# Kernel optimization log

Hardware: AMD Instinct MI355X
Metric: run time of the kernel (lower is better)

## Reference

```python
import jax, jax.numpy as jnp
import numpy as np

N_E = 50000
N_R = 1000
E = 800000
E_HIDDEN = 256
R_HIDDEN = 64
NEG_SLOPE = 0.01  # torch F.leaky_relu default


def segment_softmax(logits, seg, num_segments):
    # numerically stable per-segment softmax over edges
    seg_max = jax.ops.segment_max(logits, seg, num_segments=num_segments)
    seg_max = jnp.where(jnp.isfinite(seg_max), seg_max, 0.0)
    ex = jnp.exp(logits - seg_max[seg])
    denom = jax.ops.segment_sum(ex, seg, num_segments=num_segments)
    return ex / (denom[seg] + 1e-16)


def setup_inputs() -> dict:
    key = jax.random.key(0)
    ks = jax.random.split(key, 9)
    return {
        "x_e": jax.random.normal(ks[0], (N_E, E_HIDDEN), dtype=jnp.float32),
        "x_r": jax.random.normal(ks[1], (N_R, R_HIDDEN), dtype=jnp.float32),
        "edge_index": jax.random.randint(ks[2], (2, E), 0, N_E, dtype=jnp.int64),
        "rel": jax.random.randint(ks[3], (E,), 0, N_R, dtype=jnp.int64),
        "line_graph_index": jax.random.randint(ks[4], (2, E), 0, E, dtype=jnp.int64),
        "line_graph_val": jax.random.uniform(ks[5], (E,), dtype=jnp.float32),
        "a_h_w": jax.random.normal(ks[6], (E_HIDDEN,), dtype=jnp.float32),
        "a_t_w": jax.random.normal(ks[7], (E_HIDDEN,), dtype=jnp.float32),
        "a_r_w": jax.random.normal(ks[8], (R_HIDDEN,), dtype=jnp.float32),
    }


def reference(x_e, x_r, edge_index, rel, line_graph_index, line_graph_val, a_h_w, a_t_w, a_r_w):
    head, tail = edge_index[0], edge_index[1]
    # per-node scalar scores, gathered per edge
    s_e_h = jnp.einsum("nd,d->n", x_e, a_h_w)  # [N_e]
    s_e_t = jnp.einsum("nd,d->n", x_e, a_t_w)  # [N_e]
    s_r = jnp.einsum("rd,d->r", x_r, a_r_w)    # [N_r]
    e_h = s_e_h[head]
    e_t = s_e_t[tail]
    e_r = s_r[rel]

    n_e = x_e.shape[0]
    msg = x_r[rel]  # [E, r_hidden]

    # head branch: segment softmax over head groups, scatter-aggregate x_r[rel]
    alpha_h = segment_softmax(jax.nn.leaky_relu(e_h + e_r, NEG_SLOPE), head, n_e)
    x_e_h = jax.ops.segment_sum(alpha_h[:, None] * msg, head, num_segments=n_e)

    # tail branch: softmax grouped by tail, but spmm still scatters into head rows
    alpha_t = segment_softmax(jax.nn.leaky_relu(e_t + e_r, NEG_SLOPE), tail, n_e)
    x_e_t = jax.ops.segment_sum(alpha_t[:, None] * msg, tail, num_segments=n_e)

    return jnp.concatenate([x_e_h, x_e_t], axis=1)  # [N_e, 2*r_hidden]
```

## Files before the change

### kernel.cpp

```cpp
#include <hip/hip_runtime.h>

static constexpr int kNE = 50000;
static constexpr int kNR = 1000;
static constexpr int kE  = 800000;
static constexpr int kEH = 256;
static constexpr int kRH = 64;
static constexpr float kNeg = 0.01f;

static constexpr int kSegsPerB = 64;
static constexpr int kSegs = 2 * kNE;
static constexpr int kB = (kSegs + kSegsPerB - 1) / kSegsPerB;
static constexpr int kCap = 1536;
static constexpr int kEdgesPerBin = 4096;
static constexpr int kBinBlocks  = (kE + kEdgesPerBin - 1) / kEdgesPerBin;
static constexpr int kNodeBlocks = kNE / 8;
static constexpr int kRelBlocks  = kNR / 8;
static constexpr int kCntPad = 2048;

__device__ __forceinline__ float lrelu(float x){ return x > 0.f ? x : kNeg * x; }

__global__ __launch_bounds__(512) void k_bin_scores(
        const float* __restrict__ xe, const float* __restrict__ ahw,
        const float* __restrict__ atw, const float* __restrict__ xr,
        const float* __restrict__ arw,
        const int* __restrict__ head, const int* __restrict__ tail,
        const int* __restrict__ rel,
        float* __restrict__ s_h, float* __restrict__ s_t, float* __restrict__ s_r,
        int* __restrict__ bucket_fill, unsigned short* __restrict__ records){
    __shared__ int cnt[kCntPad];
    __shared__ int cur[kCntPad];
    __shared__ unsigned int srt[2 * kEdgesPerBin];
    __shared__ int wsum[8];

    int blk = blockIdx.x;
    int tid = threadIdx.x;
    int lane = tid & 63;

    if (blk >= kBinBlocks){
        int sb = blk - kBinBlocks;
        if (sb < kNodeBlocks){
            int node = sb * 8 + (tid >> 6);
            const float4* row = (const float4*)(xe + (size_t)node * kEH);
            float4 xv = row[lane];
            float4 av = ((const float4*)ahw)[lane];
            float4 bv = ((const float4*)atw)[lane];
            float ph = xv.x*av.x + xv.y*av.y + xv.z*av.z + xv.w*av.w;
            float pt = xv.x*bv.x + xv.y*bv.y + xv.z*bv.z + xv.w*bv.w;
            #pragma unroll
            for (int o = 32; o > 0; o >>= 1){
                ph += __shfl_down(ph, o, 64);
                pt += __shfl_down(pt, o, 64);
            }
            if (lane == 0){ s_h[node] = ph; s_t[node] = pt; }
        } else {
            int r = (sb - kNodeBlocks) * 8 + (tid >> 6);
            float p = xr[(size_t)r * kRH + lane] * arw[lane];
            #pragma unroll
            for (int o = 32; o > 0; o >>= 1) p += __shfl_down(p, o, 64);
            if (lane == 0) s_r[r] = p;
        }
        return;
    }

    int e0 = blk * kEdgesPerBin;
    for (int i = tid; i < kCntPad; i += 512) cnt[i] = 0;
    __syncthreads();

    unsigned int recs[16];
    #pragma unroll
    for (int p = 0; p < 8; ++p){
        int e = e0 + p * 512 + tid;
        unsigned int rh = 0xFFFFFFFFu, rt = 0xFFFFFFFFu;
        if (e < kE){
            int h = head[e], t = tail[e], r = rel[e];
            rh = ((unsigned int)h << 10) | (unsigned int)r;
            rt = ((unsigned int)(kNE + t) << 10) | (unsigned int)r;
            atomicAdd(&cnt[rh >> 16], 1);
            atomicAdd(&cnt[rt >> 16], 1);
        }
        recs[p] = rh; recs[8 + p] = rt;
    }
    __syncthreads();

    int c0 = cnt[4 * tid], c1 = cnt[4 * tid + 1], c2 = cnt[4 * tid + 2], c3 = cnt[4 * tid + 3];
    int v = c0 + c1 + c2 + c3;
    int x = v;
    #pragma unroll
    for (int o = 1; o < 64; o <<= 1){
        int y = __shfl_up(x, o, 64);
        if (lane >= o) x += y;
    }
    int wv = tid >> 6;
    if (lane == 63) wsum[wv] = x;
    __syncthreads();
    int wpre = 0, tot = 0;
    #pragma unroll
    for (int w = 0; w < 8; ++w){
        int s = wsum[w];
        if (w < wv) wpre += s;
        tot += s;
    }
    int base = wpre + x - v;
    cur[4 * tid]     = base;
    cur[4 * tid + 1] = base + c0;
    cur[4 * tid + 2] = base + c0 + c1;
    cur[4 * tid + 3] = base + c0 + c1 + c2;
    __syncthreads();

    #pragma unroll
    for (int p = 0; p < 16; ++p){
        unsigned int rc = recs[p];
        if (rc != 0xFFFFFFFFu){
            int slot = atomicAdd(&cur[rc >> 16], 1);
            srt[slot] = rc;
        }
    }
    __syncthreads();

    for (int i = tid; i < kB; i += 512){
        int c = cnt[i];
        if (c > 0){
            int gb = atomicAdd(&bucket_fill[i], c);
            cur[i] = gb - (cur[i] - c);
        }
    }
    __syncthreads();

    for (int j = tid; j < tot; j += 512){
        unsigned int rc = srt[j];
        int bk = rc >> 16;
        int g  = cur[bk] + j;
        if (g < kCap) records[(size_t)bk * kCap + g] = (unsigned short)(rc & 0xFFFFu);
    }
}

__global__ __launch_bounds__(256) void k_sort_aggregate(
        const int* __restrict__ bucket_fill, const unsigned short* __restrict__ records,
        const float* __restrict__ s_h, const float* __restrict__ s_t,
        const float* __restrict__ s_r, const float* __restrict__ xr,
        float* __restrict__ out){
    __shared__ float srl[kNR];
    __shared__ float sn[kSegsPerB];
    __shared__ unsigned short relbuf[kCap];
    __shared__ float alphabuf[kCap];
    __shared__ int cnt[kSegsPerB], start[kSegsPerB], cur[kSegsPerB];

    int b = blockIdx.x;
    int tid = threadIdx.x;

    for (int i = tid; i < kNR; i += 256) srl[i] = s_r[i];
    if (tid < kSegsPerB){
        cnt[tid] = 0;
        int gseg = b * kSegsPerB + tid;
        float s = 0.f;
        if (gseg < kNE) s = s_h[gseg];
        else if (gseg < kSegs) s = s_t[gseg - kNE];
        sn[tid] = s;
    }
    __syncthreads();

    int nrec = bucket_fill[b];
    if (nrec > kCap) nrec = kCap;
    const unsigned short* rb = records + (size_t)b * kCap;

    unsigned short recs[6];
    #pragma unroll
    for (int p = 0; p < 6; ++p){
        int idx = p * 256 + tid;
        unsigned short rc = 0xFFFFu;
        if (idx < nrec){
            rc = rb[idx];
            atomicAdd(&cnt[rc >> 10], 1);
        }
        recs[p] = rc;
    }
    __syncthreads();
    if (tid < kSegsPerB){
        int c = cnt[tid];
        int x = c;
        #pragma unroll
        for (int o = 1; o < 64; o <<= 1){
            int y = __shfl_up(x, o, 64);
            if (tid >= o) x += y;
        }
        int s = x - c;
        start[tid] = s;
        cur[tid] = s;
    }
    __syncthreads();
    #pragma unroll
    for (int p = 0; p < 6; ++p){
        unsigned short rc = recs[p];
        if (rc != 0xFFFFu){
            int ls = rc >> 10;
            int rr = rc & 1023;
            int slot = atomicAdd(&cur[ls], 1);
            relbuf[slot] = (unsigned short)rr;
            alphabuf[slot] = lrelu(sn[ls] + srl[rr]);
        }
    }
    __syncthreads();

    int grp = tid >> 4;
    int sub = tid & 15;
    for (int ls = grp; ls < kSegsPerB; ls += 16){
        int gseg = b * kSegsPerB + ls;
        if (gseg >= kSegs) break;
        int deg = cnt[ls], st = start[ls];

        float part = -INFINITY;
        for (int k = sub; k < deg; k += 16) part = fmaxf(part, alphabuf[st + k]);
        #pragma unroll
        for (int o = 1; o < 16; o <<= 1) part = fmaxf(part, __shfl_xor(part, o, 64));
        float m = part;

        float ss = 0.f;
        for (int k = sub; k < deg; k += 16){
            float e = __expf(alphabuf[st + k] - m);
            alphabuf[st + k] = e;
            ss += e;
        }
        #pragma unroll
        for (int o = 1; o < 16; o <<= 1) ss += __shfl_xor(ss, o, 64);
        float inv = 1.f / (ss + 1e-16f);

        float4 acc = {0.f, 0.f, 0.f, 0.f};
        int k = 0;
        for (; k + 4 <= deg; k += 4){
            int r0 = relbuf[st + k],     r1 = relbuf[st + k + 1];
            int r2 = relbuf[st + k + 2], r3 = relbuf[st + k + 3];
            float a0 = alphabuf[st + k] * inv,     a1 = alphabuf[st + k + 1] * inv;
            float a2 = alphabuf[st + k + 2] * inv, a3 = alphabuf[st + k + 3] * inv;
            float4 v0 = ((const float4*)(xr + (size_t)r0 * kRH))[sub];
            float4 v1 = ((const float4*)(xr + (size_t)r1 * kRH))[sub];
            float4 v2 = ((const float4*)(xr + (size_t)r2 * kRH))[sub];
            float4 v3 = ((const float4*)(xr + (size_t)r3 * kRH))[sub];
            acc.x += a0*v0.x + a1*v1.x + a2*v2.x + a3*v3.x;
            acc.y += a0*v0.y + a1*v1.y + a2*v2.y + a3*v3.y;
            acc.z += a0*v0.z + a1*v1.z + a2*v2.z + a3*v3.z;
            acc.w += a0*v0.w + a1*v1.w + a2*v2.w + a3*v3.w;
        }
        for (; k < deg; ++k){
            int rr = relbuf[st + k];
            float a = alphabuf[st + k] * inv;
            float4 v = ((const float4*)(xr + (size_t)rr * kRH))[sub];
            acc.x += a*v.x; acc.y += a*v.y; acc.z += a*v.z; acc.w += a*v.w;
        }
        bool isHead = gseg < kNE;
        int node = isHead ? gseg : gseg - kNE;
        float4* op = (float4*)(out + (size_t)node * (2 * kRH) + (isHead ? 0 : kRH));
        op[sub] = acc;
    }
}

extern "C" void kernel_launch(void* const* d_in, const int* in_sizes, int n_in,
                              void* d_out, int out_size, void* d_ws, size_t ws_size,
                              hipStream_t stream) {
    const float* xe  = (const float*)d_in[0];
    const float* xr  = (const float*)d_in[1];
    const int* edge_index = (const int*)d_in[2];
    const int* rel        = (const int*)d_in[3];
    const float* ahw = (const float*)d_in[6];
    const float* atw = (const float*)d_in[7];
    const float* arw = (const float*)d_in[8];
    float* out = (float*)d_out;

    const int* head = edge_index;
    const int* tail = edge_index + kE;

    char* ws = (char*)d_ws;
    float* s_h  = (float*)ws;                    ws += kNE * sizeof(float);
    float* s_t  = (float*)ws;                    ws += kNE * sizeof(float);
    float* s_r  = (float*)ws;                    ws += kNR * sizeof(float);
    int*   bucket_fill = (int*)ws;               ws += ((kB + 255) & ~255) * sizeof(int);
    unsigned short* records = (unsigned short*)ws; ws += (size_t)kB * kCap * sizeof(unsigned short);

    hipMemsetAsync(bucket_fill, 0, kB * sizeof(int), stream);
    k_bin_scores<<<kBinBlocks + kNodeBlocks + kRelBlocks, 512, 0, stream>>>(
        xe, ahw, atw, xr, arw, head, tail, rel, s_h, s_t, s_r, bucket_fill, records);
    k_sort_aggregate<<<kB, 256, 0, stream>>>(bucket_fill, records, s_h, s_t, s_r, xr, out);
}
```

Before: 159.6 us.

## Fuse binning and aggregation into one persistent kernel with grid barrier

Merges the binning/score kernel and the sort-aggregate kernel into a single persistent kernel of 256 blocks that synchronises through a global atomic barrier and flag. Each block bins a contiguous edge range, computes node and relation scores in a grid-stride loop, waits at the barrier, then processes buckets in a grid-stride loop using reused shared memory. This removes a kernel launch and the gap between the two phases. In exchange, parallelism drops to 256 blocks, and correctness depends on all blocks being co-resident so the spin barrier cannot deadlock.

```diff
diff --git a/kernel.cpp b/kernel.cpp
--- a/kernel.cpp
+++ b/kernel.cpp
@@ -11,35 +11,61 @@
 static constexpr int kSegs = 2 * kNE;
 static constexpr int kB = (kSegs + kSegsPerB - 1) / kSegsPerB;
 static constexpr int kCap = 1536;
-static constexpr int kEdgesPerBin = 4096;
-static constexpr int kBinBlocks  = (kE + kEdgesPerBin - 1) / kEdgesPerBin;
-static constexpr int kNodeBlocks = kNE / 8;
-static constexpr int kRelBlocks  = kNR / 8;
+static constexpr int kGrid = 256;
+static constexpr int kThr  = 512;
+static constexpr int kEdgesPerBlk = (kE + kGrid - 1) / kGrid;
+static constexpr int kRecsPerBlk  = 2 * kEdgesPerBlk;
 static constexpr int kCntPad = 2048;
 
 __device__ __forceinline__ float lrelu(float x){ return x > 0.f ? x : kNeg * x; }
 
-__global__ __launch_bounds__(512) void k_bin_scores(
+static constexpr int kSmemBytes = 41472;
+
+__global__ __launch_bounds__(kThr, 2) void k_fused(
         const float* __restrict__ xe, const float* __restrict__ ahw,
         const float* __restrict__ atw, const float* __restrict__ xr,
         const float* __restrict__ arw,
         const int* __restrict__ head, const int* __restrict__ tail,
         const int* __restrict__ rel,
         float* __restrict__ s_h, float* __restrict__ s_t, float* __restrict__ s_r,
-        int* __restrict__ bucket_fill, unsigned short* __restrict__ records){
-    __shared__ int cnt[kCntPad];
-    __shared__ int cur[kCntPad];
-    __shared__ unsigned int srt[2 * kEdgesPerBin];
+        int* __restrict__ bucket_fill, unsigned short* __restrict__ records,
+        int* __restrict__ bar, int* __restrict__ flag,
+        float* __restrict__ out){
+    __shared__ __align__(16) unsigned char smem[kSmemBytes];
     __shared__ int wsum[8];
 
-    int blk = blockIdx.x;
-    int tid = threadIdx.x;
+    int* cnt = (int*)smem;
+    int* cur = (int*)(smem + 8192);
+    unsigned int* srt = (unsigned int*)(smem + 16384);
+
+    int tid  = threadIdx.x;
     int lane = tid & 63;
-
-    if (blk >= kBinBlocks){
-        int sb = blk - kBinBlocks;
-        if (sb < kNodeBlocks){
-            int node = sb * 8 + (tid >> 6);
+    int wave = tid >> 6;
+
+    for (int i = tid; i < kCntPad; i += kThr) cnt[i] = 0;
+    __syncthreads();
+
+    int e0 = blockIdx.x * kEdgesPerBlk;
+    int eend = min(kE, e0 + kEdgesPerBlk);
+
+    unsigned int recs[14];
+    #pragma unroll
+    for (int p = 0; p < 7; ++p){
+        int e = e0 + p * kThr + tid;
+        unsigned int rh = 0xFFFFFFFFu, rt = 0xFFFFFFFFu;
+        if (e < eend){
+            int h = head[e], t = tail[e], r = rel[e];
+            rh = ((unsigned int)h << 10) | (unsigned int)r;
+            rt = ((unsigned int)(kNE + t) << 10) | (unsigned int)r;
+            atomicAdd(&cnt[rh >> 16], 1);
+            atomicAdd(&cnt[rt >> 16], 1);
+        }
+        recs[p] = rh; recs[7 + p] = rt;
+    }
+
+    {
+        int gw = blockIdx.x * 8 + wave;
+        for (int node = gw; node < kNE; node += kGrid * 8){
             const float4* row = (const float4*)(xe + (size_t)node * kEH);
             float4 xv = row[lane];
             float4 av = ((const float4*)ahw)[lane];
@@ -52,33 +78,13 @@
                 pt += __shfl_down(pt, o, 64);
             }
             if (lane == 0){ s_h[node] = ph; s_t[node] = pt; }
-        } else {
-            int r = (sb - kNodeBlocks) * 8 + (tid >> 6);
+        }
+        for (int r = gw; r < kNR; r += kGrid * 8){
             float p = xr[(size_t)r * kRH + lane] * arw[lane];
             #pragma unroll
             for (int o = 32; o > 0; o >>= 1) p += __shfl_down(p, o, 64);
             if (lane == 0) s_r[r] = p;
         }
-        return;
-    }
-
-    int e0 = blk * kEdgesPerBin;
-    for (int i = tid; i < kCntPad; i += 512) cnt[i] = 0;
-    __syncthreads();
-
-    unsigned int recs[16];
-    #pragma unroll
-    for (int p = 0; p < 8; ++p){
-        int e = e0 + p * 512 + tid;
-        unsigned int rh = 0xFFFFFFFFu, rt = 0xFFFFFFFFu;
-        if (e < kE){
-            int h = head[e], t = tail[e], r = rel[e];
-            rh = ((unsigned int)h << 10) | (unsigned int)r;
-            rt = ((unsigned int)(kNE + t) << 10) | (unsigned int)r;
-            atomicAdd(&cnt[rh >> 16], 1);
-            atomicAdd(&cnt[rt >> 16], 1);
-        }
-        recs[p] = rh; recs[8 + p] = rt;
     }
     __syncthreads();
 
@@ -90,14 +96,13 @@
         int y = __shfl_up(x, o, 64);
         if (lane >= o) x += y;
     }
-    int wv = tid >> 6;
-    if (lane == 63) wsum[wv] = x;
+    if (lane == 63) wsum[wave] = x;
     __syncthreads();
     int wpre = 0, tot = 0;
     #pragma unroll
     for (int w = 0; w < 8; ++w){
         int s = wsum[w];
-        if (w < wv) wpre += s;
+        if (w < wave) wpre += s;
         tot += s;
     }
     int base = wpre + x - v;
@@ -108,7 +113,7 @@
     __syncthreads();
 
     #pragma unroll
-    for (int p = 0; p < 16; ++p){
+    for (int p = 0; p < 14; ++p){
         unsigned int rc = recs[p];
         if (rc != 0xFFFFFFFFu){
             int slot = atomicAdd(&cur[rc >> 16], 1);
@@ -117,7 +122,7 @@
     }
     __syncthreads();
 
-    for (int i = tid; i < kB; i += 512){
+    for (int i = tid; i < kB; i += kThr){
         int c = cnt[i];
         if (c > 0){
             int gb = atomicAdd(&bucket_fill[i], c);
@@ -126,130 +131,141 @@
     }
     __syncthreads();
 
-    for (int j = tid; j < tot; j += 512){
+    for (int j = tid; j < tot; j += kThr){
         unsigned int rc = srt[j];
         int bk = rc >> 16;
         int g  = cur[bk] + j;
         if (g < kCap) records[(size_t)bk * kCap + g] = (unsigned short)(rc & 0xFFFFu);
     }
-}
-
-__global__ __launch_bounds__(256) void k_sort_aggregate(
-        const int* __restrict__ bucket_fill, const unsigned short* __restrict__ records,
-        const float* __restrict__ s_h, const float* __restrict__ s_t,
-        const float* __restrict__ s_r, const float* __restrict__ xr,
-        float* __restrict__ out){
-    __shared__ float srl[kNR];
-    __shared__ float sn[kSegsPerB];
-    __shared__ unsigned short relbuf[kCap];
-    __shared__ float alphabuf[kCap];
-    __shared__ int cnt[kSegsPerB], start[kSegsPerB], cur[kSegsPerB];
-
-    int b = blockIdx.x;
-    int tid = threadIdx.x;
-
-    for (int i = tid; i < kNR; i += 256) srl[i] = s_r[i];
-    if (tid < kSegsPerB){
-        cnt[tid] = 0;
-        int gseg = b * kSegsPerB + tid;
-        float s = 0.f;
-        if (gseg < kNE) s = s_h[gseg];
-        else if (gseg < kSegs) s = s_t[gseg - kNE];
-        sn[tid] = s;
-    }
-    __syncthreads();
-
-    int nrec = bucket_fill[b];
-    if (nrec > kCap) nrec = kCap;
-    const unsigned short* rb = records + (size_t)b * kCap;
-
-    unsigned short recs[6];
-    #pragma unroll
-    for (int p = 0; p < 6; ++p){
-        int idx = p * 256 + tid;
-        unsigned short rc = 0xFFFFu;
-        if (idx < nrec){
-            rc = rb[idx];
-            atomicAdd(&cnt[rc >> 10], 1);
-        }
-        recs[p] = rc;
-    }
-    __syncthreads();
-    if (tid < kSegsPerB){
-        int c = cnt[tid];
-        int x = c;
+
+    __syncthreads();
+    if (tid == 0){
+        __threadfence();
+        int prev = atomicAdd(bar, 1);
+        if (prev == (int)gridDim.x - 1){
+            __threadfence();
+            atomicExch(flag, 1);
+        } else {
+            while (atomicAdd(flag, 0) == 0){ __builtin_amdgcn_s_sleep(8); }
+        }
+        __threadfence();
+    }
+    __syncthreads();
+
+    float* srl   = (float*)smem;
+    float* sn    = (float*)(smem + 4096);
+    int* cnt2    = (int*)(smem + 4352);
+    int* start2  = (int*)(smem + 4608);
+    int* cur2    = (int*)(smem + 4864);
+    unsigned short* relbuf = (unsigned short*)(smem + 5120);
+    float* alphabuf = (float*)(smem + 8192);
+
+    for (int i = tid; i < kNR; i += kThr) srl[i] = s_r[i];
+
+    for (int bk = blockIdx.x; bk < kB; bk += kGrid){
+        __syncthreads();
+        if (tid < kSegsPerB){
+            cnt2[tid] = 0;
+            int gseg = bk * kSegsPerB + tid;
+            float s = 0.f;
+            if (gseg < kNE) s = s_h[gseg];
+            else if (gseg < kSegs) s = s_t[gseg - kNE];
+            sn[tid] = s;
+        }
+        __syncthreads();
+
+        int nrec = bucket_fill[bk];
+        if (nrec > kCap) nrec = kCap;
+        const unsigned short* rb = records + (size_t)bk * kCap;
+
+        unsigned short rr3[3];
         #pragma unroll
-        for (int o = 1; o < 64; o <<= 1){
-            int y = __shfl_up(x, o, 64);
-            if (tid >= o) x += y;
-        }
-        int s = x - c;
-        start[tid] = s;
-        cur[tid] = s;
-    }
-    __syncthreads();
-    #pragma unroll
-    for (int p = 0; p < 6; ++p){
-        unsigned short rc = recs[p];
-        if (rc != 0xFFFFu){
-            int ls = rc >> 10;
-            int rr = rc & 1023;
-            int slot = atomicAdd(&cur[ls], 1);
-            relbuf[slot] = (unsigned short)rr;
-            alphabuf[slot] = lrelu(sn[ls] + srl[rr]);
-        }
-    }
-    __syncthreads();
-
-    int grp = tid >> 4;
-    int sub = tid & 15;
-    for (int ls = grp; ls < kSegsPerB; ls += 16){
-        int gseg = b * kSegsPerB + ls;
-        if (gseg >= kSegs) break;
-        int deg = cnt[ls], st = start[ls];
-
-        float part = -INFINITY;
-        for (int k = sub; k < deg; k += 16) part = fmaxf(part, alphabuf[st + k]);
+        for (int p = 0; p < 3; ++p){
+            int idx = p * kThr + tid;
+            unsigned short rc = 0xFFFFu;
+            if (idx < nrec){
+                rc = rb[idx];
+                atomicAdd(&cnt2[rc >> 10], 1);
+            }
+            rr3[p] = rc;
+        }
+        __syncthreads();
+        if (tid < kSegsPerB){
+            int c = cnt2[tid];
+            int xx = c;
+            #pragma unroll
+            for (int o = 1; o < 64; o <<= 1){
+                int y = __shfl_up(xx, o, 64);
+                if (tid >= o) xx += y;
+            }
+            int s = xx - c;
+            start2[tid] = s;
+            cur2[tid] = s;
+        }
+        __syncthreads();
         #pragma unroll
-        for (int o = 1; o < 16; o <<= 1) part = fmaxf(part, __shfl_xor(part, o, 64));
-        float m = part;
-
-        float ss = 0.f;
-        for (int k = sub; k < deg; k += 16){
-            float e = __expf(alphabuf[st + k] - m);
-            alphabuf[st + k] = e;
-            ss += e;
-        }
-        #pragma unroll
-        for (int o = 1; o < 16; o <<= 1) ss += __shfl_xor(ss, o, 64);
-        float inv = 1.f / (ss + 1e-16f);
-
-        float4 acc = {0.f, 0.f, 0.f, 0.f};
-        int k = 0;
-        for (; k + 4 <= deg; k += 4){
-            int r0 = relbuf[st + k],     r1 = relbuf[st + k + 1];
-            int r2 = relbuf[st + k + 2], r3 = relbuf[st + k + 3];
-            float a0 = alphabuf[st + k] * inv,     a1 = alphabuf[st + k + 1] * inv;
-            float a2 = alphabuf[st + k + 2] * inv, a3 = alphabuf[st + k + 3] * inv;
-            float4 v0 = ((const float4*)(xr + (size_t)r0 * kRH))[sub];
-            float4 v1 = ((const float4*)(xr + (size_t)r1 * kRH))[sub];
-            float4 v2 = ((const float4*)(xr + (size_t)r2 * kRH))[sub];
-            float4 v3 = ((const float4*)(xr + (size_t)r3 * kRH))[sub];
-            acc.x += a0*v0.x + a1*v1.x + a2*v2.x + a3*v3.x;
-            acc.y += a0*v0.y + a1*v1.y + a2*v2.y + a3*v3.y;
-            acc.z += a0*v0.z + a1*v1.z + a2*v2.z + a3*v3.z;
-            acc.w += a0*v0.w + a1*v1.w + a2*v2.w + a3*v3.w;
-        }
-        for (; k < deg; ++k){
-            int rr = relbuf[st + k];
-            float a = alphabuf[st + k] * inv;
-            float4 v = ((const float4*)(xr + (size_t)rr * kRH))[sub];
-            acc.x += a*v.x; acc.y += a*v.y; acc.z += a*v.z; acc.w += a*v.w;
-        }
-        bool isHead = gseg < kNE;
-        int node = isHead ? gseg : gseg - kNE;
-        float4* op = (float4*)(out + (size_t)node * (2 * kRH) + (isHead ? 0 : kRH));
-        op[sub] = acc;
+        for (int p = 0; p < 3; ++p){
+            unsigned short rc = rr3[p];
+            if (rc != 0xFFFFu){
+                int ls = rc >> 10;
+                int rv = rc & 1023;
+                int slot = atomicAdd(&cur2[ls], 1);
+                relbuf[slot] = (unsigned short)rv;
+                alphabuf[slot] = lrelu(sn[ls] + srl[rv]);
+            }
+        }
+        __syncthreads();
+
+        int grp = tid >> 4;
+        int sub = tid & 15;
+        for (int ls = grp; ls < kSegsPerB; ls += 32){
+            int gseg = bk * kSegsPerB + ls;
+            if (gseg >= kSegs) break;
+            int deg = cnt2[ls], st = start2[ls];
+
+            float part = -INFINITY;
+            for (int k = sub; k < deg; k += 16) part = fmaxf(part, alphabuf[st + k]);
+            #pragma unroll
+            for (int o = 1; o < 16; o <<= 1) part = fmaxf(part, __shfl_xor(part, o, 64));
+            float m = part;
+
+            float ssum = 0.f;
+            for (int k = sub; k < deg; k += 16){
+                float e = __expf(alphabuf[st + k] - m);
+                alphabuf[st + k] = e;
+                ssum += e;
+            }
+            #pragma unroll
+            for (int o = 1; o < 16; o <<= 1) ssum += __shfl_xor(ssum, o, 64);
+            float inv = 1.f / (ssum + 1e-16f);
+
+            float4 acc = {0.f, 0.f, 0.f, 0.f};
+            int k = 0;
+            for (; k + 4 <= deg; k += 4){
+                int r0 = relbuf[st + k],     r1 = relbuf[st + k + 1];
+                int r2 = relbuf[st + k + 2], r3 = relbuf[st + k + 3];
+                float a0 = alphabuf[st + k] * inv,     a1 = alphabuf[st + k + 1] * inv;
+                float a2 = alphabuf[st + k + 2] * inv, a3 = alphabuf[st + k + 3] * inv;
+                float4 v0 = ((const float4*)(xr + (size_t)r0 * kRH))[sub];
+                float4 v1 = ((const float4*)(xr + (size_t)r1 * kRH))[sub];
+                float4 v2 = ((const float4*)(xr + (size_t)r2 * kRH))[sub];
+                float4 v3 = ((const float4*)(xr + (size_t)r3 * kRH))[sub];
+                acc.x += a0*v0.x + a1*v1.x + a2*v2.x + a3*v3.x;
+                acc.y += a0*v0.y + a1*v1.y + a2*v2.y + a3*v3.y;
+                acc.z += a0*v0.z + a1*v1.z + a2*v2.z + a3*v3.z;
+                acc.w += a0*v0.w + a1*v1.w + a2*v2.w + a3*v3.w;
+            }
+            for (; k < deg; ++k){
+                int rv = relbuf[st + k];
+                float a = alphabuf[st + k] * inv;
+                float4 vv = ((const float4*)(xr + (size_t)rv * kRH))[sub];
+                acc.x += a*vv.x; acc.y += a*vv.y; acc.z += a*vv.z; acc.w += a*vv.w;
+            }
+            bool isHead = gseg < kNE;
+            int node = isHead ? gseg : gseg - kNE;
+            float4* op = (float4*)(out + (size_t)node * (2 * kRH) + (isHead ? 0 : kRH));
+            op[sub] = acc;
+        }
     }
 }
 
@@ -272,11 +288,14 @@
     float* s_h  = (float*)ws;                    ws += kNE * sizeof(float);
     float* s_t  = (float*)ws;                    ws += kNE * sizeof(float);
     float* s_r  = (float*)ws;                    ws += kNR * sizeof(float);
-    int*   bucket_fill = (int*)ws;               ws += ((kB + 255) & ~255) * sizeof(int);
+    int*   bucket_fill = (int*)ws;               ws += (kB + 2) * sizeof(int);
+    int*   bar  = bucket_fill + kB;
+    int*   flag = bucket_fill + kB + 1;
+    ws = (char*)(((size_t)ws + 255) & ~(size_t)255);
     unsigned short* records = (unsigned short*)ws; ws += (size_t)kB * kCap * sizeof(unsigned short);
 
-    hipMemsetAsync(bucket_fill, 0, kB * sizeof(int), stream);
-    k_bin_scores<<<kBinBlocks + kNodeBlocks + kRelBlocks, 512, 0, stream>>>(
-        xe, ahw, atw, xr, arw, head, tail, rel, s_h, s_t, s_r, bucket_fill, records);
-    k_sort_aggregate<<<kB, 256, 0, stream>>>(bucket_fill, records, s_h, s_t, s_r, xr, out);
+    hipMemsetAsync(bucket_fill, 0, (kB + 2) * sizeof(int), stream);
+    k_fused<<<kGrid, kThr, 0, stream>>>(xe, ahw, atw, xr, arw, head, tail, rel,
+                                        s_h, s_t, s_r, bucket_fill, records,
+                                        bar, flag, out);
 }
```

After: 220.9 us. 1.38x slower.
